# Optimization experiments

Measured on AMD Instinct MI355X. Metric: run time of the kernel, lower is better.

The kernel has to match this reference:

```python
import jax, jax.numpy as jnp
import numpy as np


def setup_inputs() -> dict:
    key = jax.random.key(0)
    k1, k2, k3 = jax.random.split(key, 3)
    B, N, M, C = 4, 4096, 8192, 64
    PPU = 64.0  # points_per_unit
    xz = jax.random.normal(k1, (B, M, 1), dtype=jnp.float32) * 10.0  # grid locations
    z = jax.random.normal(k2, (B, C, M), dtype=jnp.float32)          # channels-first features
    x = jax.random.normal(k3, (B, N, 1), dtype=jnp.float32) * 10.0   # query locations
    log_scale = jnp.asarray(np.log(2.0 / PPU), dtype=jnp.float32)
    return {"xz": xz, "z": z, "x": x, "log_scale": log_scale}


def reference(xz, z, x, log_scale):
    # pairwise squared distances between x [B,N,1] and xz [B,M,1] -> [B,N,M]
    diff = x - jnp.swapaxes(xz, -1, -2)            # [B,N,M]
    dists2 = diff * diff
    # RBF weights (no normalization)
    weights = jnp.exp(-0.5 * dists2 / jnp.exp(2.0 * log_scale))  # [B,N,M]
    # z: [B,C,M] -> transpose -> [B,M,C]; weights @ z^T -> [B,N,C]
    out = jnp.einsum('bnm,bcm->bnc', weights, z)
    return out
```

## Files before the change

### kernel.cpp

```cpp
#include <hip/hip_runtime.h>
#include <math.h>

#define B 4
#define N 4096
#define M 8192
#define C 64
#define NB 2048
#define XMIN (-64.0f)
#define INV_BW 16.0f
#define CUT 10.0f
#define QG 16

typedef __attribute__((ext_vector_type(8))) short short8;
typedef __attribute__((ext_vector_type(4))) float f32x4;

__device__ __forceinline__ int bucket_of(float v) {
    int k = (int)floorf((v - XMIN) * INV_BW);
    return min(max(k, 0), NB - 1);
}

__device__ __forceinline__ unsigned short f2bf(float f) {
    unsigned int u = __float_as_uint(f);
    return (unsigned short)((u + 0x7FFF + ((u >> 16) & 1)) >> 16);
}

__global__ __launch_bounds__(1024) void bin_kernel(
    const float* __restrict__ xz, const float* __restrict__ x,
    int* __restrict__ bucket_start,
    float* __restrict__ xs,
    int* __restrict__ islot,
    float* __restrict__ qcs,
    int* __restrict__ qis)
{
    const int t    = threadIdx.x;
    const int lane = t & 63;
    const int w    = t >> 6;

    __shared__ int hist[NB];
    __shared__ int run[NB];
    __shared__ int wsum[16];
    const bool isQ = blockIdx.x >= 4;
    const int  b   = blockIdx.x & 3;
    const int  PT  = isQ ? (N / 1024) : (M / 1024);
    const float* src = isQ ? (x + b * N) : (xz + b * M);

    hist[t] = 0; hist[t + 1024] = 0;
    __syncthreads();

    float pv[8]; int pk[8];
    for (int j = 0; j < PT; ++j) {
        float v = src[j * 1024 + t];
        pv[j] = v; pk[j] = bucket_of(v);
        atomicAdd(&hist[pk[j]], 1);
    }
    __syncthreads();

    const int h0 = hist[2 * t], h1 = hist[2 * t + 1];
    const int tot = h0 + h1;
    int s = tot;
    #pragma unroll
    for (int off = 1; off < 64; off <<= 1) {
        int up = __shfl_up(s, off, 64);
        if (lane >= off) s += up;
    }
    if (lane == 63) wsum[w] = s;
    __syncthreads();
    int woff = 0;
    for (int i = 0; i < w; ++i) woff += wsum[i];
    const int excl = woff + s - tot;

    run[2 * t]     = excl;
    run[2 * t + 1] = excl + h0;
    if (!isQ) {
        bucket_start[b * (NB + 1) + 2 * t]     = excl;
        bucket_start[b * (NB + 1) + 2 * t + 1] = excl + h0;
        if (t == 1023) bucket_start[b * (NB + 1) + NB] = woff + s;
    }
    __syncthreads();

    if (!isQ) {
        for (int j = 0; j < PT; ++j) {
            int slot = atomicAdd(&run[pk[j]], 1);
            xs[b * M + slot]            = pv[j];
            islot[b * M + j * 1024 + t] = slot;
        }
    } else {
        for (int j = 0; j < PT; ++j) {
            int slot = atomicAdd(&run[pk[j]], 1);
            qcs[b * N + slot] = pv[j];
            qis[b * N + slot] = j * 1024 + t;
        }
    }
}

__global__ __launch_bounds__(1024) void permz_kernel(
    const float* __restrict__ z, const int* __restrict__ islot,
    unsigned short* __restrict__ zs)
{
    const int t  = threadIdx.x;
    const int b  = blockIdx.x >> 7;
    const int m0 = (blockIdx.x & 127) * 64;
    __shared__ float tile[64][65];
    __shared__ int slot_s[64];

    const int m = t & 63;
    #pragma unroll
    for (int k = 0; k < 4; ++k) {
        int c = (t >> 6) + 16 * k;
        tile[c][m] = z[((size_t)b * C + c) * M + m0 + m];
    }
    if (t < 64) slot_s[t] = islot[b * M + m0 + t];
    __syncthreads();

    const int j  = t >> 4;
    const int c4 = t & 15;
    ushort4 v4;
    v4.x = f2bf(tile[c4 * 4 + 0][j]);
    v4.y = f2bf(tile[c4 * 4 + 1][j]);
    v4.z = f2bf(tile[c4 * 4 + 2][j]);
    v4.w = f2bf(tile[c4 * 4 + 3][j]);
    ((ushort4*)zs)[((size_t)b * M + slot_s[j]) * 16 + c4] = v4;
}

__global__ __launch_bounds__(256) void gather_kernel(
    const float* __restrict__ log_scale,
    const int* __restrict__ bucket_start,
    const float* __restrict__ xs,
    const float* __restrict__ qcs,
    const int* __restrict__ qis,
    const unsigned short* __restrict__ zs,
    float* __restrict__ out)
{
    const int t    = threadIdx.x;
    const int lane = t & 63;
    const int w    = t >> 6;
    const int quad = lane >> 4;
    const int low4 = lane & 15;
    const int g  = blockIdx.x;
    const int b  = g >> 8;
    const int g0 = (g & 255) * QG;

    __shared__ unsigned short zr[64 * 64];
    __shared__ unsigned short wl[QG][72];
    __shared__ float qcS[QG];
    __shared__ int   qiS[QG];

    const float ls   = log_scale[0];
    const float coef = -0.5f * __expf(-2.0f * ls);
    const float R    = sqrtf(CUT / (-coef));

    if (t < QG) {
        qcS[t] = qcs[b * N + g0 + t];
        qiS[t] = qis[b * N + g0 + t];
    }
    __syncthreads();

    float xmin = qcS[0], xmax = qcS[0];
    #pragma unroll
    for (int j = 1; j < QG; ++j) {
        xmin = fminf(xmin, qcS[j]);
        xmax = fmaxf(xmax, qcS[j]);
    }
    const int s0 = bucket_start[b * (NB + 1) + bucket_of(xmin - R)];
    const int s1 = bucket_start[b * (NB + 1) + bucket_of(xmax + R) + 1];
    const int e0 = s0 & ~63;
    const int e1 = (s1 + 63) & ~63;

    const int qw = w * 4 + (lane >> 4);
    const int pg = lane & 15;
    const float qv = qcS[qw];

    f32x4 acc = {0.f, 0.f, 0.f, 0.f};

    const float* xsb = xs + b * M;
    const unsigned short* zsb = zs + (size_t)b * M * C;

    for (int cs = e0; cs < e1; cs += 64) {
        __syncthreads();
        #pragma unroll
        for (int r = 0; r < 2; ++r) {
            const unsigned short* gp =
                zsb + ((size_t)cs + (w * 2 + r) * 8 + (lane >> 3)) * C + (lane & 7) * 8;
            unsigned short* lp = zr + (w * 2 + r) * 512;
            __builtin_amdgcn_global_load_lds(
                (const __attribute__((address_space(1))) void*)gp,
                (__attribute__((address_space(3))) void*)lp, 16, 0, 0);
        }
        {
            const float4 xp4 = *(const float4*)(xsb + cs + pg * 4);
            float d0 = qv - xp4.x, d1 = qv - xp4.y;
            float d2 = qv - xp4.z, d3 = qv - xp4.w;
            ushort4 wv;
            wv.x = f2bf(__expf(coef * d0 * d0));
            wv.y = f2bf(__expf(coef * d1 * d1));
            wv.z = f2bf(__expf(coef * d2 * d2));
            wv.w = f2bf(__expf(coef * d3 * d3));
            *(ushort4*)&wl[qw][pg * 4] = wv;
        }
        __syncthreads();
        #pragma unroll
        for (int kh = 0; kh < 2; ++kh) {
            short8 afrag = *(const short8*)&wl[low4][kh * 32 + quad * 8];
            short8 bfrag;
            #pragma unroll
            for (int j = 0; j < 8; ++j) {
                const int p = kh * 32 + quad * 8 + j;
                bfrag[j] = (short)zr[p * 64 + w * 16 + low4];
            }
            acc = __builtin_amdgcn_mfma_f32_16x16x32_bf16(afrag, bfrag, acc, 0, 0, 0);
        }
    }

    #pragma unroll
    for (int r = 0; r < 4; ++r) {
        const int q = quad * 4 + r;
        out[((size_t)b * N + qiS[q]) * C + w * 16 + low4] = acc[r];
    }
}

extern "C" void kernel_launch(void* const* d_in, const int* in_sizes, int n_in,
                              void* d_out, int out_size, void* d_ws, size_t ws_size,
                              hipStream_t stream) {
    const float* xz = (const float*)d_in[0];
    const float* z  = (const float*)d_in[1];
    const float* x  = (const float*)d_in[2];
    const float* ls = (const float*)d_in[3];
    float* out = (float*)d_out;

    char* ws = (char*)d_ws;
    size_t off = 0;
    auto alloc = [&](size_t bytes) { void* p = ws + off; off += (bytes + 255) & ~size_t(255); return p; };

    unsigned short* zs = (unsigned short*)alloc(((size_t)B * M + 64) * C * sizeof(unsigned short));
    float* xs    = (float*)alloc(((size_t)B * M + 64) * sizeof(float));
    int*   islot = (int*)alloc((size_t)B * M * sizeof(int));
    float* qcs   = (float*)alloc((size_t)B * N * sizeof(float));
    int*   qis   = (int*)alloc((size_t)B * N * sizeof(int));
    int*   bst   = (int*)alloc((size_t)B * (NB + 1) * sizeof(int));

    bin_kernel<<<8, 1024, 0, stream>>>(xz, x, bst, xs, islot, qcs, qis);
    permz_kernel<<<512, 1024, 0, stream>>>(z, islot, zs);
    gather_kernel<<<B * (N / QG), 256, 0, stream>>>(ls, bst, xs, qcs, qis, zs, out);
}
```

Baseline: 83.91 us.

## Store sorted z channel-major with XOR swizzle and double-buffer gather stages

The permute kernel now gathers z through an inverse-order index (sorted slot to original point) and writes each 64-point chunk in a channel-major, XOR-swizzled bf16 layout. The gather kernel can then load B fragments as a single 16-byte LDS read instead of eight scalar loads. The gather loop is also double-buffered, staging the next chunk's async loads and weights while the current MFMAs run, and the block index is swizzled across batches. The costs are twice the LDS use and reads of z from scattered addresses in the permute kernel.

```diff
diff --git a/kernel.cpp b/kernel.cpp
--- a/kernel.cpp
+++ b/kernel.cpp
@@ -28,7 +28,7 @@
     const float* __restrict__ xz, const float* __restrict__ x,
     int* __restrict__ bucket_start,
     float* __restrict__ xs,
-    int* __restrict__ islot,
+    int* __restrict__ iord,
     float* __restrict__ qcs,
     int* __restrict__ qis)
 {
@@ -81,8 +81,8 @@
     if (!isQ) {
         for (int j = 0; j < PT; ++j) {
             int slot = atomicAdd(&run[pk[j]], 1);
-            xs[b * M + slot]            = pv[j];
-            islot[b * M + j * 1024 + t] = slot;
+            xs[b * M + slot]   = pv[j];
+            iord[b * M + slot] = j * 1024 + t;
         }
     } else {
         for (int j = 0; j < PT; ++j) {
@@ -93,33 +93,31 @@
     }
 }
 
-__global__ __launch_bounds__(1024) void permz_kernel(
-    const float* __restrict__ z, const int* __restrict__ islot,
+__global__ __launch_bounds__(256) void permz_kernel(
+    const float* __restrict__ z, const int* __restrict__ iord,
     unsigned short* __restrict__ zs)
 {
-    const int t  = threadIdx.x;
-    const int b  = blockIdx.x >> 7;
-    const int m0 = (blockIdx.x & 127) * 64;
-    __shared__ float tile[64][65];
-    __shared__ int slot_s[64];
-
-    const int m = t & 63;
-    #pragma unroll
-    for (int k = 0; k < 4; ++k) {
-        int c = (t >> 6) + 16 * k;
-        tile[c][m] = z[((size_t)b * C + c) * M + m0 + m];
-    }
-    if (t < 64) slot_s[t] = islot[b * M + m0 + t];
-    __syncthreads();
-
-    const int j  = t >> 4;
-    const int c4 = t & 15;
-    ushort4 v4;
-    v4.x = f2bf(tile[c4 * 4 + 0][j]);
-    v4.y = f2bf(tile[c4 * 4 + 1][j]);
-    v4.z = f2bf(tile[c4 * 4 + 2][j]);
-    v4.w = f2bf(tile[c4 * 4 + 3][j]);
-    ((ushort4*)zs)[((size_t)b * M + slot_s[j]) * 16 + c4] = v4;
+    const int t    = threadIdx.x;
+    const int lane = t & 63;
+    const int w    = t >> 6;
+    const int b    = blockIdx.x >> 7;
+    const int ck   = blockIdx.x & 127;
+
+    const int m = iord[b * M + ck * 64 + lane];
+    const float* zb = z + (size_t)b * C * M;
+    unsigned short* dst = zs + ((size_t)b * 128 + ck) * 4096;
+    const int blk = lane >> 3;
+    const int lo  = lane & 7;
+
+    float v[16];
+    #pragma unroll
+    for (int k = 0; k < 16; ++k)
+        v[k] = zb[(size_t)(w * 16 + k) * M + m];
+    #pragma unroll
+    for (int k = 0; k < 16; ++k) {
+        const int c = w * 16 + k;
+        dst[c * 64 + (((blk ^ (c & 7)) << 3) | lo)] = f2bf(v[k]);
+    }
 }
 
 __global__ __launch_bounds__(256) void gather_kernel(
@@ -136,12 +134,13 @@
     const int w    = t >> 6;
     const int quad = lane >> 4;
     const int low4 = lane & 15;
-    const int g  = blockIdx.x;
-    const int b  = g >> 8;
-    const int g0 = (g & 255) * QG;
-
-    __shared__ unsigned short zr[64 * 64];
-    __shared__ unsigned short wl[QG][72];
+    const int gid = blockIdx.x;
+    const int swz = (gid & 7) * 128 + (gid >> 3);
+    const int b   = swz >> 8;
+    const int g0  = (swz & 255) * QG;
+
+    __shared__ unsigned short zr[2][64 * 64];
+    __shared__ unsigned short wl[2][QG][72];
     __shared__ float qcS[QG];
     __shared__ int   qiS[QG];
 
@@ -165,50 +164,54 @@
     const int s1 = bucket_start[b * (NB + 1) + bucket_of(xmax + R) + 1];
     const int e0 = s0 & ~63;
     const int e1 = (s1 + 63) & ~63;
-
-    const int qw = w * 4 + (lane >> 4);
-    const int pg = lane & 15;
+    const int nck = (e1 - e0) >> 6;
+
+    const int qw  = w * 4 + quad;
+    const int pg  = low4;
     const float qv = qcS[qw];
+    const int row = w * 16 + low4;
+
+    const float* xsb = xs + b * M;
+    const unsigned short* zcb = zs + (size_t)b * M * C;
 
     f32x4 acc = {0.f, 0.f, 0.f, 0.f};
 
-    const float* xsb = xs + b * M;
-    const unsigned short* zsb = zs + (size_t)b * M * C;
-
-    for (int cs = e0; cs < e1; cs += 64) {
-        __syncthreads();
+    auto STAGE_W = [&](int i, int p) {
+        const unsigned short* gsrc =
+            zcb + ((size_t)((e0 >> 6) + i)) * 4096 + (w * 2) * 512 + lane * 8;
+        __builtin_amdgcn_global_load_lds(
+            (const __attribute__((address_space(1))) void*)gsrc,
+            (__attribute__((address_space(3))) void*)(&zr[p][(w * 2) * 512]),
+            16, 0, 0);
+        __builtin_amdgcn_global_load_lds(
+            (const __attribute__((address_space(1))) void*)(gsrc + 512),
+            (__attribute__((address_space(3))) void*)(&zr[p][(w * 2 + 1) * 512]),
+            16, 0, 0);
+        const float4 xp4 = *(const float4*)(xsb + e0 + i * 64 + pg * 4);
+        float d0 = qv - xp4.x, d1 = qv - xp4.y;
+        float d2 = qv - xp4.z, d3 = qv - xp4.w;
+        ushort4 wv;
+        wv.x = f2bf(__expf(coef * d0 * d0));
+        wv.y = f2bf(__expf(coef * d1 * d1));
+        wv.z = f2bf(__expf(coef * d2 * d2));
+        wv.w = f2bf(__expf(coef * d3 * d3));
+        *(ushort4*)&wl[p][qw][pg * 4] = wv;
+    };
+
+    if (nck > 0) STAGE_W(0, 0);
+    __syncthreads();
+
+    for (int i = 0; i < nck; ++i) {
+        const int cur = i & 1;
+        if (i + 1 < nck) STAGE_W(i + 1, cur ^ 1);
         #pragma unroll
-        for (int r = 0; r < 2; ++r) {
-            const unsigned short* gp =
-                zsb + ((size_t)cs + (w * 2 + r) * 8 + (lane >> 3)) * C + (lane & 7) * 8;
-            unsigned short* lp = zr + (w * 2 + r) * 512;
-            __builtin_amdgcn_global_load_lds(
-                (const __attribute__((address_space(1))) void*)gp,
-                (__attribute__((address_space(3))) void*)lp, 16, 0, 0);
-        }
-        {
-            const float4 xp4 = *(const float4*)(xsb + cs + pg * 4);
-            float d0 = qv - xp4.x, d1 = qv - xp4.y;
-            float d2 = qv - xp4.z, d3 = qv - xp4.w;
-            ushort4 wv;
-            wv.x = f2bf(__expf(coef * d0 * d0));
-            wv.y = f2bf(__expf(coef * d1 * d1));
-            wv.z = f2bf(__expf(coef * d2 * d2));
-            wv.w = f2bf(__expf(coef * d3 * d3));
-            *(ushort4*)&wl[qw][pg * 4] = wv;
+        for (int kh = 0; kh < 2; ++kh) {
+            short8 afrag = *(const short8*)&wl[cur][low4][kh * 32 + quad * 8];
+            short8 bfrag = *(const short8*)
+                &zr[cur][row * 64 + (((kh * 4 + quad) ^ (row & 7)) << 3)];
+            acc = __builtin_amdgcn_mfma_f32_16x16x32_bf16(afrag, bfrag, acc, 0, 0, 0);
         }
         __syncthreads();
-        #pragma unroll
-        for (int kh = 0; kh < 2; ++kh) {
-            short8 afrag = *(const short8*)&wl[low4][kh * 32 + quad * 8];
-            short8 bfrag;
-            #pragma unroll
-            for (int j = 0; j < 8; ++j) {
-                const int p = kh * 32 + quad * 8 + j;
-                bfrag[j] = (short)zr[p * 64 + w * 16 + low4];
-            }
-            acc = __builtin_amdgcn_mfma_f32_16x16x32_bf16(afrag, bfrag, acc, 0, 0, 0);
-        }
     }
 
     #pragma unroll
@@ -231,14 +234,14 @@
     size_t off = 0;
     auto alloc = [&](size_t bytes) { void* p = ws + off; off += (bytes + 255) & ~size_t(255); return p; };
 
-    unsigned short* zs = (unsigned short*)alloc(((size_t)B * M + 64) * C * sizeof(unsigned short));
-    float* xs    = (float*)alloc(((size_t)B * M + 64) * sizeof(float));
-    int*   islot = (int*)alloc((size_t)B * M * sizeof(int));
+    unsigned short* zs = (unsigned short*)alloc((size_t)B * M * C * sizeof(unsigned short));
+    float* xs    = (float*)alloc((size_t)B * M * sizeof(float));
+    int*   iord  = (int*)alloc((size_t)B * M * sizeof(int));
     float* qcs   = (float*)alloc((size_t)B * N * sizeof(float));
     int*   qis   = (int*)alloc((size_t)B * N * sizeof(int));
     int*   bst   = (int*)alloc((size_t)B * (NB + 1) * sizeof(int));
 
-    bin_kernel<<<8, 1024, 0, stream>>>(xz, x, bst, xs, islot, qcs, qis);
-    permz_kernel<<<512, 1024, 0, stream>>>(z, islot, zs);
+    bin_kernel<<<8, 1024, 0, stream>>>(xz, x, bst, xs, iord, qcs, qis);
+    permz_kernel<<<512, 256, 0, stream>>>(z, iord, zs);
     gather_kernel<<<B * (N / QG), 256, 0, stream>>>(ls, bst, xs, qcs, qis, zs, out);
 }
```

Result: slower. 95.27 us (+13.5%).

## Pre-transpose z into swizzled chunks and double-buffer a wider gather tile

Applied to the files above, without the earlier changes.

A new kernel transposes the sorted bf16 z rows into per-64-point channel-major chunks with an XOR swizzle. This lets the gather kernel read MFMA B fragments as single 16-byte LDS loads instead of eight scalar, bank-conflicted reads. The gather kernel now handles 32 queries per 512-thread block, halving redundant z chunk traffic per query. It double-buffers the z and weight staging so the next chunk loads while the current one computes, and it reorders block indices. The cost is an extra launch plus one more full pass over z through the workspace.

```diff
diff --git a/kernel.cpp b/kernel.cpp
--- a/kernel.cpp
+++ b/kernel.cpp
@@ -9,7 +9,7 @@
 #define XMIN (-64.0f)
 #define INV_BW 16.0f
 #define CUT 10.0f
-#define QG 16
+#define QG2 32
 
 typedef __attribute__((ext_vector_type(8))) short short8;
 typedef __attribute__((ext_vector_type(4))) float f32x4;
@@ -95,7 +95,7 @@
 
 __global__ __launch_bounds__(1024) void permz_kernel(
     const float* __restrict__ z, const int* __restrict__ islot,
-    unsigned short* __restrict__ zs)
+    unsigned short* __restrict__ zrow)
 {
     const int t  = threadIdx.x;
     const int b  = blockIdx.x >> 7;
@@ -119,10 +119,34 @@
     v4.y = f2bf(tile[c4 * 4 + 1][j]);
     v4.z = f2bf(tile[c4 * 4 + 2][j]);
     v4.w = f2bf(tile[c4 * 4 + 3][j]);
-    ((ushort4*)zs)[((size_t)b * M + slot_s[j]) * 16 + c4] = v4;
-}
-
-__global__ __launch_bounds__(256) void gather_kernel(
+    ((ushort4*)zrow)[((size_t)b * M + slot_s[j]) * 16 + c4] = v4;
+}
+
+__global__ __launch_bounds__(256) void transp_kernel(
+    const unsigned short* __restrict__ zrow,
+    unsigned short* __restrict__ zs)
+{
+    const int t   = threadIdx.x;
+    const int b   = blockIdx.x >> 7;
+    const int ck  = blockIdx.x & 127;
+    const int c   = t >> 2;
+    const int seg = t & 3;
+
+    const unsigned short* src = zrow + ((size_t)(b * M + ck * 64)) * 64 + c;
+    unsigned short* dst = zs + ((size_t)b * 128 + ck) * 4096 + c * 64;
+
+    #pragma unroll
+    for (int h = 0; h < 2; ++h) {
+        const int pb = seg * 2 + h;
+        short8 v;
+        #pragma unroll
+        for (int j = 0; j < 8; ++j)
+            v[j] = (short)src[(size_t)(pb * 8 + j) * 64];
+        *(short8*)(dst + (((pb ^ (c & 7)) << 3))) = v;
+    }
+}
+
+__global__ __launch_bounds__(512) void gather_kernel(
     const float* __restrict__ log_scale,
     const int* __restrict__ bucket_start,
     const float* __restrict__ xs,
@@ -136,20 +160,23 @@
     const int w    = t >> 6;
     const int quad = lane >> 4;
     const int low4 = lane & 15;
-    const int g  = blockIdx.x;
-    const int b  = g >> 8;
-    const int g0 = (g & 255) * QG;
-
-    __shared__ unsigned short zr[64 * 64];
-    __shared__ unsigned short wl[QG][72];
-    __shared__ float qcS[QG];
-    __shared__ int   qiS[QG];
+    const int qt   = w >> 2;
+    const int ct   = w & 3;
+    const int gid = blockIdx.x;
+    const int swz = (gid & 7) * 64 + (gid >> 3);
+    const int b   = swz >> 7;
+    const int g0  = (swz & 127) * QG2;
+
+    __shared__ unsigned short zr[2][64 * 64];
+    __shared__ unsigned short wl[2][QG2][72];
+    __shared__ float qcS[QG2];
+    __shared__ int   qiS[QG2];
 
     const float ls   = log_scale[0];
     const float coef = -0.5f * __expf(-2.0f * ls);
     const float R    = sqrtf(CUT / (-coef));
 
-    if (t < QG) {
+    if (t < QG2) {
         qcS[t] = qcs[b * N + g0 + t];
         qiS[t] = qis[b * N + g0 + t];
     }
@@ -157,7 +184,7 @@
 
     float xmin = qcS[0], xmax = qcS[0];
     #pragma unroll
-    for (int j = 1; j < QG; ++j) {
+    for (int j = 1; j < QG2; ++j) {
         xmin = fminf(xmin, qcS[j]);
         xmax = fmaxf(xmax, qcS[j]);
     }
@@ -165,56 +192,56 @@
     const int s1 = bucket_start[b * (NB + 1) + bucket_of(xmax + R) + 1];
     const int e0 = s0 & ~63;
     const int e1 = (s1 + 63) & ~63;
-
-    const int qw = w * 4 + (lane >> 4);
-    const int pg = lane & 15;
+    const int nck = (e1 - e0) >> 6;
+
+    const int qw  = w * 4 + quad;
+    const int pg  = low4;
     const float qv = qcS[qw];
+    const int row = ct * 16 + low4;
+
+    const float* xsb = xs + b * M;
+    const unsigned short* zcb = zs + (size_t)b * M * C;
 
     f32x4 acc = {0.f, 0.f, 0.f, 0.f};
 
-    const float* xsb = xs + b * M;
-    const unsigned short* zsb = zs + (size_t)b * M * C;
-
-    for (int cs = e0; cs < e1; cs += 64) {
-        __syncthreads();
+    auto STAGE_W = [&](int i, int p) {
+        const unsigned short* gsrc =
+            zcb + ((size_t)((e0 >> 6) + i)) * 4096 + w * 512 + lane * 8;
+        __builtin_amdgcn_global_load_lds(
+            (const __attribute__((address_space(1))) void*)gsrc,
+            (__attribute__((address_space(3))) void*)(&zr[p][w * 512]),
+            16, 0, 0);
+        const float4 xp4 = *(const float4*)(xsb + e0 + i * 64 + pg * 4);
+        float d0 = qv - xp4.x, d1 = qv - xp4.y;
+        float d2 = qv - xp4.z, d3 = qv - xp4.w;
+        ushort4 wv;
+        wv.x = f2bf(__expf(coef * d0 * d0));
+        wv.y = f2bf(__expf(coef * d1 * d1));
+        wv.z = f2bf(__expf(coef * d2 * d2));
+        wv.w = f2bf(__expf(coef * d3 * d3));
+        *(ushort4*)&wl[p][qw][pg * 4] = wv;
+    };
+
+    if (nck > 0) STAGE_W(0, 0);
+    __syncthreads();
+
+    for (int i = 0; i < nck; ++i) {
+        const int cur = i & 1;
+        if (i + 1 < nck) STAGE_W(i + 1, cur ^ 1);
         #pragma unroll
-        for (int r = 0; r < 2; ++r) {
-            const unsigned short* gp =
-                zsb + ((size_t)cs + (w * 2 + r) * 8 + (lane >> 3)) * C + (lane & 7) * 8;
-            unsigned short* lp = zr + (w * 2 + r) * 512;
-            __builtin_amdgcn_global_load_lds(
-                (const __attribute__((address_space(1))) void*)gp,
-                (__attribute__((address_space(3))) void*)lp, 16, 0, 0);
-        }
-        {
-            const float4 xp4 = *(const float4*)(xsb + cs + pg * 4);
-            float d0 = qv - xp4.x, d1 = qv - xp4.y;
-            float d2 = qv - xp4.z, d3 = qv - xp4.w;
-            ushort4 wv;
-            wv.x = f2bf(__expf(coef * d0 * d0));
-            wv.y = f2bf(__expf(coef * d1 * d1));
-            wv.z = f2bf(__expf(coef * d2 * d2));
-            wv.w = f2bf(__expf(coef * d3 * d3));
-            *(ushort4*)&wl[qw][pg * 4] = wv;
+        for (int kh = 0; kh < 2; ++kh) {
+            short8 afrag = *(const short8*)&wl[cur][qt * 16 + low4][kh * 32 + quad * 8];
+            short8 bfrag = *(const short8*)
+                &zr[cur][row * 64 + (((kh * 4 + quad) ^ (row & 7)) << 3)];
+            acc = __builtin_amdgcn_mfma_f32_16x16x32_bf16(afrag, bfrag, acc, 0, 0, 0);
         }
         __syncthreads();
-        #pragma unroll
-        for (int kh = 0; kh < 2; ++kh) {
-            short8 afrag = *(const short8*)&wl[low4][kh * 32 + quad * 8];
-            short8 bfrag;
-            #pragma unroll
-            for (int j = 0; j < 8; ++j) {
-                const int p = kh * 32 + quad * 8 + j;
-                bfrag[j] = (short)zr[p * 64 + w * 16 + low4];
-            }
-            acc = __builtin_amdgcn_mfma_f32_16x16x32_bf16(afrag, bfrag, acc, 0, 0, 0);
-        }
     }
 
     #pragma unroll
     for (int r = 0; r < 4; ++r) {
-        const int q = quad * 4 + r;
-        out[((size_t)b * N + qiS[q]) * C + w * 16 + low4] = acc[r];
+        const int q = qt * 16 + quad * 4 + r;
+        out[((size_t)b * N + qiS[q]) * C + ct * 16 + low4] = acc[r];
     }
 }
 
@@ -231,7 +258,8 @@
     size_t off = 0;
     auto alloc = [&](size_t bytes) { void* p = ws + off; off += (bytes + 255) & ~size_t(255); return p; };
 
-    unsigned short* zs = (unsigned short*)alloc(((size_t)B * M + 64) * C * sizeof(unsigned short));
+    unsigned short* zrow = (unsigned short*)alloc(((size_t)B * M + 64) * C * sizeof(unsigned short));
+    unsigned short* zs   = (unsigned short*)alloc((size_t)B * M * C * sizeof(unsigned short));
     float* xs    = (float*)alloc(((size_t)B * M + 64) * sizeof(float));
     int*   islot = (int*)alloc((size_t)B * M * sizeof(int));
     float* qcs   = (float*)alloc((size_t)B * N * sizeof(float));
@@ -239,6 +267,7 @@
     int*   bst   = (int*)alloc((size_t)B * (NB + 1) * sizeof(int));
 
     bin_kernel<<<8, 1024, 0, stream>>>(xz, x, bst, xs, islot, qcs, qis);
-    permz_kernel<<<512, 1024, 0, stream>>>(z, islot, zs);
-    gather_kernel<<<B * (N / QG), 256, 0, stream>>>(ls, bst, xs, qcs, qis, zs, out);
-}
+    permz_kernel<<<512, 1024, 0, stream>>>(z, islot, zrow);
+    transp_kernel<<<512, 256, 0, stream>>>(zrow, zs);
+    gather_kernel<<<B * (N / QG2), 512, 0, stream>>>(ls, bst, xs, qcs, qis, zs, out);
+}
```

New measurement: 87.16 us. 1.04x slower.

## Split binning into per-chunk histogram and scatter kernels across more blocks

Applied to the files above, without the earlier changes.

Replaces the single 8-block binning kernel with two kernels: a 24-block partial histogram pass over 2048-element chunks, and a 24-block scatter pass. The scatter pass combines the partial histograms to get global bucket offsets plus each chunk's prefix before writing sorted positions. This spreads the serial binning work over three times as many blocks and uses vectorised float4 loads. In exchange it adds a kernel launch and a global round trip through the partial histograms.

```diff
diff --git a/kernel.cpp b/kernel.cpp
--- a/kernel.cpp
+++ b/kernel.cpp
@@ -10,6 +10,8 @@
 #define INV_BW 16.0f
 #define CUT 10.0f
 #define QG 16
+#define NSUBP 4
+#define NSUBQ 2
 
 typedef __attribute__((ext_vector_type(8))) short short8;
 typedef __attribute__((ext_vector_type(4))) float f32x4;
@@ -24,8 +26,38 @@
     return (unsigned short)((u + 0x7FFF + ((u >> 16) & 1)) >> 16);
 }
 
-__global__ __launch_bounds__(1024) void bin_kernel(
+__global__ __launch_bounds__(256) void hist_kernel(
     const float* __restrict__ xz, const float* __restrict__ x,
+    int* __restrict__ part)
+{
+    const int t   = threadIdx.x;
+    const int bid = blockIdx.x;
+    __shared__ int h[NB];
+    #pragma unroll
+    for (int i = 0; i < 8; ++i) h[t + 256 * i] = 0;
+    __syncthreads();
+
+    const bool isQ = bid >= 16;
+    const int  b   = isQ ? (bid - 16) >> 1 : bid >> 2;
+    const int  sub = isQ ? (bid - 16) & 1  : bid & 3;
+    const float* src = (isQ ? x + b * N : xz + b * M) + sub * 2048;
+
+    #pragma unroll
+    for (int j = 0; j < 2; ++j) {
+        float4 v4 = *(const float4*)(src + t * 4 + j * 1024);
+        atomicAdd(&h[bucket_of(v4.x)], 1);
+        atomicAdd(&h[bucket_of(v4.y)], 1);
+        atomicAdd(&h[bucket_of(v4.z)], 1);
+        atomicAdd(&h[bucket_of(v4.w)], 1);
+    }
+    __syncthreads();
+    #pragma unroll
+    for (int i = 0; i < 8; ++i) part[bid * NB + t + 256 * i] = h[t + 256 * i];
+}
+
+__global__ __launch_bounds__(256) void scat_kernel(
+    const float* __restrict__ xz, const float* __restrict__ x,
+    const int* __restrict__ part,
     int* __restrict__ bucket_start,
     float* __restrict__ xs,
     int* __restrict__ islot,
@@ -35,60 +67,71 @@
     const int t    = threadIdx.x;
     const int lane = t & 63;
     const int w    = t >> 6;
-
-    __shared__ int hist[NB];
-    __shared__ int run[NB];
-    __shared__ int wsum[16];
-    const bool isQ = blockIdx.x >= 4;
-    const int  b   = blockIdx.x & 3;
-    const int  PT  = isQ ? (N / 1024) : (M / 1024);
-    const float* src = isQ ? (x + b * N) : (xz + b * M);
-
-    hist[t] = 0; hist[t + 1024] = 0;
-    __syncthreads();
-
-    float pv[8]; int pk[8];
-    for (int j = 0; j < PT; ++j) {
-        float v = src[j * 1024 + t];
-        pv[j] = v; pk[j] = bucket_of(v);
-        atomicAdd(&hist[pk[j]], 1);
-    }
-    __syncthreads();
-
-    const int h0 = hist[2 * t], h1 = hist[2 * t + 1];
-    const int tot = h0 + h1;
-    int s = tot;
+    const int bid  = blockIdx.x;
+    const bool isQ = bid >= 16;
+    const int  b   = isQ ? (bid - 16) >> 1 : bid >> 2;
+    const int  sub = isQ ? (bid - 16) & 1  : bid & 3;
+    const int  nsub = isQ ? NSUBQ : NSUBP;
+    const int  pb0  = isQ ? 16 + b * 2 : b * 4;
+    const float* src = (isQ ? x + b * N : xz + b * M) + sub * 2048;
+
+    __shared__ int base[NB];
+    __shared__ int cnt[NB];
+    __shared__ int wsum[4];
+
+    int tot[8], mine[8];
+    #pragma unroll
+    for (int j = 0; j < 8; ++j) { tot[j] = 0; mine[j] = 0; }
+    for (int s_ = 0; s_ < nsub; ++s_) {
+        #pragma unroll
+        for (int j = 0; j < 8; ++j) {
+            const int v = part[(pb0 + s_) * NB + t * 8 + j];
+            tot[j] += v;
+            if (s_ < sub) mine[j] += v;
+        }
+    }
+    int pre[8]; int tsum = 0;
+    #pragma unroll
+    for (int j = 0; j < 8; ++j) { pre[j] = tsum; tsum += tot[j]; }
+    int s = tsum;
     #pragma unroll
     for (int off = 1; off < 64; off <<= 1) {
         int up = __shfl_up(s, off, 64);
         if (lane >= off) s += up;
     }
     if (lane == 63) wsum[w] = s;
+    #pragma unroll
+    for (int i = 0; i < 8; ++i) cnt[t + 256 * i] = 0;
     __syncthreads();
     int woff = 0;
     for (int i = 0; i < w; ++i) woff += wsum[i];
-    const int excl = woff + s - tot;
-
-    run[2 * t]     = excl;
-    run[2 * t + 1] = excl + h0;
-    if (!isQ) {
-        bucket_start[b * (NB + 1) + 2 * t]     = excl;
-        bucket_start[b * (NB + 1) + 2 * t + 1] = excl + h0;
-        if (t == 1023) bucket_start[b * (NB + 1) + NB] = woff + s;
-    }
-    __syncthreads();
-
-    if (!isQ) {
-        for (int j = 0; j < PT; ++j) {
-            int slot = atomicAdd(&run[pk[j]], 1);
-            xs[b * M + slot]            = pv[j];
-            islot[b * M + j * 1024 + t] = slot;
-        }
-    } else {
-        for (int j = 0; j < PT; ++j) {
-            int slot = atomicAdd(&run[pk[j]], 1);
-            qcs[b * N + slot] = pv[j];
-            qis[b * N + slot] = j * 1024 + t;
+    const int excl = woff + s - tsum;
+    #pragma unroll
+    for (int j = 0; j < 8; ++j) base[t * 8 + j] = excl + pre[j] + mine[j];
+    if (!isQ && sub == 0) {
+        #pragma unroll
+        for (int j = 0; j < 8; ++j)
+            bucket_start[b * (NB + 1) + t * 8 + j] = excl + pre[j];
+        if (t == 255) bucket_start[b * (NB + 1) + NB] = woff + s;
+    }
+    __syncthreads();
+
+    #pragma unroll
+    for (int j = 0; j < 2; ++j) {
+        float4 v4 = *(const float4*)(src + t * 4 + j * 1024);
+        float vv[4] = {v4.x, v4.y, v4.z, v4.w};
+        #pragma unroll
+        for (int c = 0; c < 4; ++c) {
+            const int k    = bucket_of(vv[c]);
+            const int slot = base[k] + atomicAdd(&cnt[k], 1);
+            const int orig = sub * 2048 + t * 4 + j * 1024 + c;
+            if (!isQ) {
+                xs[b * M + slot]    = vv[c];
+                islot[b * M + orig] = slot;
+            } else {
+                qcs[b * N + slot] = vv[c];
+                qis[b * N + slot] = orig;
+            }
         }
     }
 }
@@ -237,8 +280,10 @@
     float* qcs   = (float*)alloc((size_t)B * N * sizeof(float));
     int*   qis   = (int*)alloc((size_t)B * N * sizeof(int));
     int*   bst   = (int*)alloc((size_t)B * (NB + 1) * sizeof(int));
-
-    bin_kernel<<<8, 1024, 0, stream>>>(xz, x, bst, xs, islot, qcs, qis);
+    int*   part  = (int*)alloc((size_t)24 * NB * sizeof(int));
+
+    hist_kernel<<<24, 256, 0, stream>>>(xz, x, part);
+    scat_kernel<<<24, 256, 0, stream>>>(xz, x, part, bst, xs, islot, qcs, qis);
     permz_kernel<<<512, 1024, 0, stream>>>(z, islot, zs);
     gather_kernel<<<B * (N / QG), 256, 0, stream>>>(ls, bst, xs, qcs, qis, zs, out);
 }
```

Result: no change. 83.89 us (-0.0%).
